# Kernel tuning notes

Measured on AMD Instinct MI355X. Metric: run time of the kernel, lower is better.

Reference implementation:

```python
import jax, jax.numpy as jnp
import numpy as np

D_MODEL = 1024
NUM_HEADS = 16
D_K = D_MODEL // NUM_HEADS


def setup_inputs() -> dict:
    key = jax.random.key(0)
    ks = jax.random.split(key, 5)
    B, S = 4, 2048
    scale = 1.0 / np.sqrt(D_MODEL)
    x = jax.random.normal(ks[0], (B, S, D_MODEL), dtype=jnp.float32)
    # Linear(d_model, d_model, bias=False) weights, stored as [out, in] like torch
    Wq = jax.random.normal(ks[1], (D_MODEL, D_MODEL), dtype=jnp.float32) * scale
    Wk = jax.random.normal(ks[2], (D_MODEL, D_MODEL), dtype=jnp.float32) * scale
    Wv = jax.random.normal(ks[3], (D_MODEL, D_MODEL), dtype=jnp.float32) * scale
    Wo = jax.random.normal(ks[4], (D_MODEL, D_MODEL), dtype=jnp.float32) * scale
    return {"x": x, "Wq": Wq, "Wk": Wk, "Wv": Wv, "Wo": Wo}


def reference(x, Wq, Wk, Wv, Wo):
    B, S, D = x.shape
    H, dk = NUM_HEADS, D_K
    # projections (torch Linear: x @ W.T)
    q = (x @ Wq.T).reshape(B, S, H, dk).transpose(0, 2, 1, 3)  # [B,H,S,dk]
    k = (x @ Wk.T).reshape(B, S, H, dk).transpose(0, 2, 1, 3)
    v = (x @ Wv.T).reshape(B, S, H, dk).transpose(0, 2, 1, 3)
    scores = jnp.einsum("bhqd,bhkd->bhqk", q, k) / jnp.sqrt(jnp.float32(dk))
    causal = jnp.triu(jnp.ones((S, S), dtype=bool), k=1)  # True above diagonal -> masked
    scores = jnp.where(causal[None, None], -jnp.inf, scores)
    attn = jax.nn.softmax(scores, axis=-1)
    out = jnp.einsum("bhqk,bhkd->bhqd", attn, v)  # [B,H,S,dk]
    out = out.transpose(0, 2, 1, 3).reshape(B, S, D)
    return out @ Wo.T
```

## Files before the change

### kernel.cpp

```cpp
#include <hip/hip_runtime.h>

typedef __bf16 bf16_t;
typedef __bf16 bf16x8 __attribute__((ext_vector_type(8)));
typedef __bf16 bf16x4 __attribute__((ext_vector_type(4)));
typedef float f32x4 __attribute__((ext_vector_type(4)));
typedef unsigned short u16x8 __attribute__((ext_vector_type(8)));

#define AS1C(p) ((const __attribute__((address_space(1))) void*)(p))
#define AS3(p) ((__attribute__((address_space(3))) void*)(p))
#define MM(a, b, c) __builtin_amdgcn_mfma_f32_16x16x32_bf16(a, b, c, 0, 0, 0)

__device__ __forceinline__ unsigned short f2b_rne(float f) {
  union { float f; unsigned u; } x; x.f = f;
  unsigned u = x.u;
  u += 0x7fffu + ((u >> 16) & 1u);
  return (unsigned short)(u >> 16);
}

__device__ __forceinline__ float fast_exp2(float x) {
  return __builtin_amdgcn_exp2f(x);
}

__global__ __launch_bounds__(256) void cast_all(const float* __restrict__ x,
                                                const float* __restrict__ w0,
                                                const float* __restrict__ w1,
                                                const float* __restrict__ w2,
                                                const float* __restrict__ w3,
                                                unsigned short* __restrict__ xout,
                                                unsigned short* __restrict__ wout) {
  int bid = blockIdx.x;
  const float* in;
  unsigned short* out;
  int base;
  if (bid < 4096) {
    in = x; out = xout; base = bid * 2048;
  } else {
    int widx = (bid - 4096) >> 9;
    in = (widx == 0) ? w0 : (widx == 1) ? w1 : (widx == 2) ? w2 : w3;
    out = wout + (size_t)widx * (1024u * 1024u);
    base = ((bid - 4096) & 511) * 2048;
  }
  int i = base + threadIdx.x * 8;
  const float4* p = reinterpret_cast<const float4*>(in + i);
  float4 a = p[0], b = p[1];
  u16x8 o;
  o[0] = f2b_rne(a.x); o[1] = f2b_rne(a.y); o[2] = f2b_rne(a.z); o[3] = f2b_rne(a.w);
  o[4] = f2b_rne(b.x); o[5] = f2b_rne(b.y); o[6] = f2b_rne(b.z); o[7] = f2b_rne(b.w);
  *reinterpret_cast<u16x8*>(out + i) = o;
}

template <int OUT_F32, int NJ>
__global__ __launch_bounds__(512, 4) void gemmk(const bf16_t* __restrict__ A,
                                                const bf16_t* __restrict__ Bm,
                                                void* __restrict__ C,
                                                int M, int N, int K, int lda,
                                                float scale, int qlim) {
  constexpr int BN = NJ * 64;
  constexpr int BUFE = (128 + BN) * 32;
  extern __shared__ bf16_t lds[];
  const int tid = threadIdx.x;
  const int w = tid >> 6, l = tid & 63;
  const int r = l & 15, kg = l >> 4;
  const int wm = (w >> 2) * 64;
  const int wn = (w & 3) * (NJ * 16);
  const int m0 = blockIdx.y * 128, n0 = blockIdx.x * BN;
  const int srow = w * 16 + (l >> 2);
  const int scol = (l & 3) * 8;
  const bf16_t* aS = A + (size_t)(m0 + srow) * lda + scol;
  const bf16_t* bS = Bm + (size_t)(n0 + srow) * K + scol;

  f32x4 acc[4][NJ] = {};

  auto STAGE = [&](bf16_t* sb, int kt) {
    __builtin_amdgcn_global_load_lds(AS1C(aS + kt * 32), AS3(sb + w * 512), 16, 0, 0);
    __builtin_amdgcn_global_load_lds(AS1C(bS + kt * 32), AS3(sb + 4096 + w * 512), 16, 0, 0);
    if (NJ == 4)
      __builtin_amdgcn_global_load_lds(AS1C(bS + (size_t)128 * K + kt * 32),
                                       AS3(sb + 8192 + w * 512), 16, 0, 0);
  };

  bf16_t* cur = lds;
  bf16_t* nxt = lds + BUFE;
  bf16_t* stg = lds + 2 * BUFE;

  STAGE(cur, 0);
  STAGE(nxt, 1);
  if (NJ == 4) asm volatile("s_waitcnt vmcnt(3)" ::: "memory");
  else         asm volatile("s_waitcnt vmcnt(2)" ::: "memory");
  __builtin_amdgcn_s_barrier();

  const int NT = K >> 5;
  for (int t = 0; t < NT; ++t) {
    bf16x8 AF[4], BF[NJ];
#pragma unroll
    for (int il = 0; il < 4; ++il)
      AF[il] = *reinterpret_cast<const bf16x8*>(cur + (wm + il * 16 + r) * 32 + kg * 8);
#pragma unroll
    for (int jl = 0; jl < NJ; ++jl)
      BF[jl] = *reinterpret_cast<const bf16x8*>(cur + 4096 + (wn + jl * 16 + r) * 32 + kg * 8);
    const int kt = (t + 2 < NT) ? t + 2 : t;
    STAGE(stg, kt);
    if (NJ == 4) asm volatile("s_waitcnt lgkmcnt(2)" ::: "memory");
    else         asm volatile("s_waitcnt lgkmcnt(1)" ::: "memory");
    __builtin_amdgcn_sched_barrier(0);
    __builtin_amdgcn_s_setprio(1);
#pragma unroll
    for (int il = 0; il < 4; ++il)
#pragma unroll
      for (int jl = 0; jl < NJ / 2; ++jl)
        acc[il][jl] = MM(AF[il], BF[jl], acc[il][jl]);
    __builtin_amdgcn_s_setprio(0);
    asm volatile("s_waitcnt lgkmcnt(0)" ::: "memory");
    __builtin_amdgcn_sched_barrier(0);
    __builtin_amdgcn_s_setprio(1);
#pragma unroll
    for (int il = 0; il < 4; ++il)
#pragma unroll
      for (int jl = NJ / 2; jl < NJ; ++jl)
        acc[il][jl] = MM(AF[il], BF[jl], acc[il][jl]);
    __builtin_amdgcn_s_setprio(0);
    if (NJ == 4) asm volatile("s_waitcnt vmcnt(3)" ::: "memory");
    else         asm volatile("s_waitcnt vmcnt(2)" ::: "memory");
    __builtin_amdgcn_s_barrier();
    bf16_t* tmp = cur; cur = nxt; nxt = stg; stg = tmp;
  }

#pragma unroll
  for (int il = 0; il < 4; ++il)
#pragma unroll
    for (int jl = 0; jl < NJ; ++jl) {
      const int row0 = m0 + wm + il * 16 + kg * 4;
      const int col = n0 + wn + jl * 16 + r;
      const float sc = (col < qlim) ? scale : 1.0f;
#pragma unroll
      for (int v = 0; v < 4; ++v) {
        float val = acc[il][jl][v] * sc;
        size_t idx = (size_t)(row0 + v) * N + col;
        if (OUT_F32) reinterpret_cast<float*>(C)[idx] = val;
        else reinterpret_cast<unsigned short*>(C)[idx] = f2b_rne(val);
      }
    }
}

__global__ __launch_bounds__(256) void transpose_v(const bf16_t* __restrict__ qkv,
                                                   bf16_t* __restrict__ vt) {
  __shared__ bf16_t Vs[64 * 72];
  const int t = threadIdx.x;
  const int s0 = blockIdx.x * 64;
  const int bh = blockIdx.y;
  const int b = bh >> 4, h = bh & 15;
  const size_t in_base = ((size_t)b * 2048 + s0) * 3072 + 2048 + h * 64;
#pragma unroll
  for (int c = 0; c < 2; ++c) {
    int chunk = c * 256 + t;
    int ss = chunk >> 3, dd = (chunk & 7) * 8;
    bf16x8 v = *reinterpret_cast<const bf16x8*>(qkv + in_base + (size_t)ss * 3072 + dd);
    *reinterpret_cast<bf16x8*>(Vs + ss * 72 + dd) = v;
  }
  __syncthreads();
  const size_t out_base = (size_t)bh * 64 * 2048 + s0;
#pragma unroll
  for (int c = 0; c < 2; ++c) {
    int chunk = c * 256 + t;
    int dd = chunk >> 3, ss = (chunk & 7) * 8;
    bf16x8 o;
#pragma unroll
    for (int j = 0; j < 8; ++j) o[j] = Vs[(ss + j) * 72 + dd];
    *reinterpret_cast<bf16x8*>(vt + out_base + (size_t)dd * 2048 + ss) = o;
  }
}

__global__ __launch_bounds__(512, 4) void flash_attn(const bf16_t* __restrict__ QKV,
                                                     const bf16_t* __restrict__ VT,
                                                     unsigned short* __restrict__ O,
                                                     int ostride) {
  __shared__ bf16_t Ks[2][64 * 72];
  __shared__ bf16_t Vts[2][64 * 72];
  __shared__ bf16_t Pl[8][2][16 * 68];
  const int tid = threadIdx.x;
  const int lane = tid & 63, wave = tid >> 6;
  const int r = lane & 15, kg = lane >> 4;
  const int bh = blockIdx.x;
  const int y = blockIdx.y;
  const int pair = (y < 4) ? y : 11 - y;
  const int b = bh >> 4, h = bh & 15;
  const size_t qkv_row0 = (size_t)b * 2048 * 3072;
  const int qcol = h * 64, kcol = 1024 + h * 64;
  const size_t vt_base = (size_t)bh * 64 * 2048;
  const size_t o_row0 = (size_t)b * 2048 * ostride;
  const int ocol = h * 64;
  const int srr = tid >> 3, scc = (tid & 7) * 8;

  const int q0L = pair * 128, q0H = (15 - pair) * 128;
  const int qrowL = q0L + wave * 16 + r, qrowH = q0H + wave * 16 + r;
  const int tmaxL = (q0L + wave * 16 + 15) >> 6;
  const int tmaxH = (q0H + wave * 16 + 15) >> 6;
  const int NT = 32 - 2 * pair;

  const size_t qoffL = qkv_row0 + (size_t)qrowL * 3072 + qcol;
  const size_t qoffH = qkv_row0 + (size_t)qrowH * 3072 + qcol;
  bf16x8 qfL0 = *reinterpret_cast<const bf16x8*>(QKV + qoffL + kg * 8);
  bf16x8 qfL1 = *reinterpret_cast<const bf16x8*>(QKV + qoffL + 32 + kg * 8);
  bf16x8 qfH0 = *reinterpret_cast<const bf16x8*>(QKV + qoffH + kg * 8);
  bf16x8 qfH1 = *reinterpret_cast<const bf16x8*>(QKV + qoffH + 32 + kg * 8);

  f32x4 oaccL[4] = {}, oaccH[4] = {};
  float mL = -3e30f, lL = 0.f, mH = -3e30f, lH = 0.f;

  bf16x8 gk = *reinterpret_cast<const bf16x8*>(QKV + qkv_row0 + (size_t)srr * 3072 + kcol + scc);
  bf16x8 gv = *reinterpret_cast<const bf16x8*>(VT + vt_base + (size_t)srr * 2048 + scc);

  for (int t = 0; t < NT; ++t) {
    const int buf = t & 1;
    *reinterpret_cast<bf16x8*>(&Ks[buf][srr * 72 + scc]) = gk;
    *reinterpret_cast<bf16x8*>(&Vts[buf][srr * 72 + scc]) = gv;
    __syncthreads();
    if (t + 1 < NT) {
      const int kv1 = (t + 1) * 64;
      gk = *reinterpret_cast<const bf16x8*>(QKV + qkv_row0 + (size_t)(kv1 + srr) * 3072 + kcol + scc);
      gv = *reinterpret_cast<const bf16x8*>(VT + vt_base + (size_t)srr * 2048 + kv1 + scc);
    }
    if (t > tmaxH) continue;

    const int kv0 = t * 64;
    const bool doL = (t <= tmaxL);

    bf16x8 kf[4][2];
#pragma unroll
    for (int nt = 0; nt < 4; ++nt) {
      kf[nt][0] = *reinterpret_cast<const bf16x8*>(&Ks[buf][(nt * 16 + r) * 72 + kg * 8]);
      kf[nt][1] = *reinterpret_cast<const bf16x8*>(&Ks[buf][(nt * 16 + r) * 72 + 32 + kg * 8]);
    }
    float valsL[16], valsH[16];
    __builtin_amdgcn_s_setprio(1);
    if (doL) {
#pragma unroll
      for (int nt = 0; nt < 4; ++nt) {
        f32x4 sL = {};
        sL = MM(kf[nt][0], qfL0, sL);
        sL = MM(kf[nt][1], qfL1, sL);
#pragma unroll
        for (int v = 0; v < 4; ++v) valsL[nt * 4 + v] = sL[v];
      }
    }
#pragma unroll
    for (int nt = 0; nt < 4; ++nt) {
      f32x4 sH = {};
      sH = MM(kf[nt][0], qfH0, sH);
      sH = MM(kf[nt][1], qfH1, sH);
#pragma unroll
      for (int v = 0; v < 4; ++v) valsH[nt * 4 + v] = sH[v];
    }
    __builtin_amdgcn_s_setprio(0);

    if (doL) {
      if (t == tmaxL) {
#pragma unroll
        for (int nt = 0; nt < 4; ++nt)
#pragma unroll
          for (int v = 0; v < 4; ++v)
            if (kv0 + nt * 16 + kg * 4 + v > qrowL) valsL[nt * 4 + v] = -3e30f;
      }
      float a0 = fmaxf(fmaxf(valsL[0], valsL[1]), valsL[2]);
      float a1 = fmaxf(fmaxf(valsL[3], valsL[4]), valsL[5]);
      float a2 = fmaxf(fmaxf(valsL[6], valsL[7]), valsL[8]);
      float a3 = fmaxf(fmaxf(valsL[9], valsL[10]), valsL[11]);
      float a4 = fmaxf(fmaxf(valsL[12], valsL[13]), valsL[14]);
      float pmax = fmaxf(fmaxf(fmaxf(a0, a1), fmaxf(a2, a3)), fmaxf(a4, valsL[15]));
      if (!__all(pmax <= mL + 8.0f)) {
        pmax = fmaxf(pmax, __shfl_xor(pmax, 16));
        pmax = fmaxf(pmax, __shfl_xor(pmax, 32));
        const float m_new = fmaxf(mL, pmax);
        const float alpha = fast_exp2(mL - m_new);
        lL *= alpha;
        f32x4 al;
#pragma unroll
        for (int v = 0; v < 4; ++v) al[v] = __shfl(alpha, kg * 4 + v);
#pragma unroll
        for (int dt = 0; dt < 4; ++dt)
#pragma unroll
          for (int v = 0; v < 4; ++v) oaccL[dt][v] *= al[v];
        mL = m_new;
      }
#pragma unroll
      for (int ii = 0; ii < 16; ++ii) {
        float p = fast_exp2(valsL[ii] - mL);
        valsL[ii] = p;
        lL += p;
      }
#pragma unroll
      for (int nt = 0; nt < 4; ++nt) {
        bf16x4 pb;
#pragma unroll
        for (int v = 0; v < 4; ++v) pb[v] = (bf16_t)valsL[nt * 4 + v];
        *reinterpret_cast<bf16x4*>(&Pl[wave][0][r * 68 + nt * 16 + kg * 4]) = pb;
      }
      bf16x8 pa0 = *reinterpret_cast<const bf16x8*>(&Pl[wave][0][r * 68 + kg * 8]);
      bf16x8 pa1 = *reinterpret_cast<const bf16x8*>(&Pl[wave][0][r * 68 + 32 + kg * 8]);
#pragma unroll
      for (int dt = 0; dt < 4; ++dt) {
        bf16x8 vb0 = *reinterpret_cast<const bf16x8*>(&Vts[buf][(dt * 16 + r) * 72 + kg * 8]);
        bf16x8 vb1 = *reinterpret_cast<const bf16x8*>(&Vts[buf][(dt * 16 + r) * 72 + 32 + kg * 8]);
        oaccL[dt] = MM(pa0, vb0, oaccL[dt]);
        oaccL[dt] = MM(pa1, vb1, oaccL[dt]);
      }
    }

    {
      if (t == tmaxH) {
#pragma unroll
        for (int nt = 0; nt < 4; ++nt)
#pragma unroll
          for (int v = 0; v < 4; ++v)
            if (kv0 + nt * 16 + kg * 4 + v > qrowH) valsH[nt * 4 + v] = -3e30f;
      }
      float a0 = fmaxf(fmaxf(valsH[0], valsH[1]), valsH[2]);
      float a1 = fmaxf(fmaxf(valsH[3], valsH[4]), valsH[5]);
      float a2 = fmaxf(fmaxf(valsH[6], valsH[7]), valsH[8]);
      float a3 = fmaxf(fmaxf(valsH[9], valsH[10]), valsH[11]);
      float a4 = fmaxf(fmaxf(valsH[12], valsH[13]), valsH[14]);
      float pmax = fmaxf(fmaxf(fmaxf(a0, a1), fmaxf(a2, a3)), fmaxf(a4, valsH[15]));
      if (!__all(pmax <= mH + 8.0f)) {
        pmax = fmaxf(pmax, __shfl_xor(pmax, 16));
        pmax = fmaxf(pmax, __shfl_xor(pmax, 32));
        const float m_new = fmaxf(mH, pmax);
        const float alpha = fast_exp2(mH - m_new);
        lH *= alpha;
        f32x4 al;
#pragma unroll
        for (int v = 0; v < 4; ++v) al[v] = __shfl(alpha, kg * 4 + v);
#pragma unroll
        for (int dt = 0; dt < 4; ++dt)
#pragma unroll
          for (int v = 0; v < 4; ++v) oaccH[dt][v] *= al[v];
        mH = m_new;
      }
#pragma unroll
      for (int ii = 0; ii < 16; ++ii) {
        float p = fast_exp2(valsH[ii] - mH);
        valsH[ii] = p;
        lH += p;
      }
#pragma unroll
      for (int nt = 0; nt < 4; ++nt) {
        bf16x4 pb;
#pragma unroll
        for (int v = 0; v < 4; ++v) pb[v] = (bf16_t)valsH[nt * 4 + v];
        *reinterpret_cast<bf16x4*>(&Pl[wave][1][r * 68 + nt * 16 + kg * 4]) = pb;
      }
      bf16x8 pa0 = *reinterpret_cast<const bf16x8*>(&Pl[wave][1][r * 68 + kg * 8]);
      bf16x8 pa1 = *reinterpret_cast<const bf16x8*>(&Pl[wave][1][r * 68 + 32 + kg * 8]);
      __builtin_amdgcn_s_setprio(1);
#pragma unroll
      for (int dt = 0; dt < 4; ++dt) {
        bf16x8 vb0 = *reinterpret_cast<const bf16x8*>(&Vts[buf][(dt * 16 + r) * 72 + kg * 8]);
        bf16x8 vb1 = *reinterpret_cast<const bf16x8*>(&Vts[buf][(dt * 16 + r) * 72 + 32 + kg * 8]);
        oaccH[dt] = MM(pa0, vb0, oaccH[dt]);
        oaccH[dt] = MM(pa1, vb1, oaccH[dt]);
      }
      __builtin_amdgcn_s_setprio(0);
    }
  }

  {
    float l_row = lL;
    l_row += __shfl_xor(l_row, 16);
    l_row += __shfl_xor(l_row, 32);
    const float linv = 1.0f / l_row;
    f32x4 il;
#pragma unroll
    for (int v = 0; v < 4; ++v) il[v] = __shfl(linv, kg * 4 + v);
    const size_t orow0 = o_row0 + (size_t)(q0L + wave * 16) * ostride + ocol;
#pragma unroll
    for (int dt = 0; dt < 4; ++dt) {
      const int d = dt * 16 + r;
#pragma unroll
      for (int v = 0; v < 4; ++v)
        O[orow0 + (size_t)(kg * 4 + v) * ostride + d] = f2b_rne(oaccL[dt][v] * il[v]);
    }
  }
  {
    float l_row = lH;
    l_row += __shfl_xor(l_row, 16);
    l_row += __shfl_xor(l_row, 32);
    const float linv = 1.0f / l_row;
    f32x4 il;
#pragma unroll
    for (int v = 0; v < 4; ++v) il[v] = __shfl(linv, kg * 4 + v);
    const size_t orow0 = o_row0 + (size_t)(q0H + wave * 16) * ostride + ocol;
#pragma unroll
    for (int dt = 0; dt < 4; ++dt) {
      const int d = dt * 16 + r;
#pragma unroll
      for (int v = 0; v < 4; ++v)
        O[orow0 + (size_t)(kg * 4 + v) * ostride + d] = f2b_rne(oaccH[dt][v] * il[v]);
    }
  }
}

extern "C" void kernel_launch(void* const* d_in, const int* in_sizes, int n_in,
                              void* d_out, int out_size, void* d_ws, size_t ws_size,
                              hipStream_t stream) {
  const float* x  = (const float*)d_in[0];
  const float* Wq = (const float*)d_in[1];
  const float* Wk = (const float*)d_in[2];
  const float* Wv = (const float*)d_in[3];
  const float* Wo = (const float*)d_in[4];

  char* ws = (char*)d_ws;
  bf16_t* xb  = (bf16_t*)(ws);
  bf16_t* wqb = (bf16_t*)(ws + (16u << 20));
  bf16_t* wob = (bf16_t*)(ws + (22u << 20));
  bf16_t* qkv = (bf16_t*)(ws + (24u << 20));
  bf16_t* vt  = (bf16_t*)(ws);

  hipFuncSetAttribute(reinterpret_cast<const void*>(&gemmk<0, 4>),
                      hipFuncAttributeMaxDynamicSharedMemorySize, 73728);
  hipFuncSetAttribute(reinterpret_cast<const void*>(&gemmk<1, 2>),
                      hipFuncAttributeMaxDynamicSharedMemorySize, 49152);

  cast_all<<<4096 + 2048, 256, 0, stream>>>(x, Wq, Wk, Wv, Wo,
                                            (unsigned short*)xb, (unsigned short*)wqb);

  gemmk<0, 4><<<dim3(3072 / 256, 8192 / 128), 512, 73728, stream>>>(
      xb, wqb, qkv, 8192, 3072, 1024, 1024, 0.18033688011112042f, 1024);

  transpose_v<<<dim3(2048 / 64, 64), 256, 0, stream>>>(qkv, vt);

  flash_attn<<<dim3(64, 8), 512, 0, stream>>>(qkv, vt, (unsigned short*)qkv, 3072);

  gemmk<1, 2><<<dim3(1024 / 128, 8192 / 128), 512, 49152, stream>>>(
      qkv, wob, d_out, 8192, 1024, 1024, 3072, 1.0f, 0);
}
```

Before: 172.9 us.

## Fuse V transpose into QKV GEMM epilogue and hoist V fragment loads

Result: slower. 219.4 us (+26.9%).

```diff
diff --git a/kernel.cpp b/kernel.cpp
--- a/kernel.cpp
+++ b/kernel.cpp
@@ -5,6 +5,7 @@
 typedef __bf16 bf16x4 __attribute__((ext_vector_type(4)));
 typedef float f32x4 __attribute__((ext_vector_type(4)));
 typedef unsigned short u16x8 __attribute__((ext_vector_type(8)));
+typedef unsigned short u16x4 __attribute__((ext_vector_type(4)));
 
 #define AS1C(p) ((const __attribute__((address_space(1))) void*)(p))
 #define AS3(p) ((__attribute__((address_space(3))) void*)(p))
@@ -53,7 +54,8 @@
 __global__ __launch_bounds__(512, 4) void gemmk(const bf16_t* __restrict__ A,
                                                 const bf16_t* __restrict__ Bm,
                                                 void* __restrict__ C,
-                                                int M, int N, int K, int lda,
+                                                bf16_t* __restrict__ vt,
+                                                int M, int ldc, int K, int lda,
                                                 float scale, int qlim) {
   constexpr int BN = NJ * 64;
   constexpr int BUFE = (128 + BN) * 32;
@@ -125,6 +127,22 @@
     bf16_t* tmp = cur; cur = nxt; nxt = stg; stg = tmp;
   }
 
+  if (!OUT_F32 && vt && n0 >= 2048) {
+#pragma unroll
+    for (int il = 0; il < 4; ++il)
+#pragma unroll
+      for (int jl = 0; jl < NJ; ++jl) {
+        const int row0 = m0 + wm + il * 16 + kg * 4;
+        const int vc = n0 + wn + jl * 16 + r - 2048;
+        const int hh = vc >> 6, dd = vc & 63;
+        const int bb = row0 >> 11, ss = row0 & 2047;
+        u16x4 pb;
+#pragma unroll
+        for (int v = 0; v < 4; ++v) pb[v] = f2b_rne(acc[il][jl][v]);
+        *reinterpret_cast<u16x4*>(vt + ((size_t)((bb * 16 + hh) * 64 + dd) << 11) + ss) = pb;
+      }
+    return;
+  }
 #pragma unroll
   for (int il = 0; il < 4; ++il)
 #pragma unroll
@@ -135,42 +153,14 @@
 #pragma unroll
       for (int v = 0; v < 4; ++v) {
         float val = acc[il][jl][v] * sc;
-        size_t idx = (size_t)(row0 + v) * N + col;
+        size_t idx = (size_t)(row0 + v) * ldc + col;
         if (OUT_F32) reinterpret_cast<float*>(C)[idx] = val;
         else reinterpret_cast<unsigned short*>(C)[idx] = f2b_rne(val);
       }
     }
 }
 
-__global__ __launch_bounds__(256) void transpose_v(const bf16_t* __restrict__ qkv,
-                                                   bf16_t* __restrict__ vt) {
-  __shared__ bf16_t Vs[64 * 72];
-  const int t = threadIdx.x;
-  const int s0 = blockIdx.x * 64;
-  const int bh = blockIdx.y;
-  const int b = bh >> 4, h = bh & 15;
-  const size_t in_base = ((size_t)b * 2048 + s0) * 3072 + 2048 + h * 64;
-#pragma unroll
-  for (int c = 0; c < 2; ++c) {
-    int chunk = c * 256 + t;
-    int ss = chunk >> 3, dd = (chunk & 7) * 8;
-    bf16x8 v = *reinterpret_cast<const bf16x8*>(qkv + in_base + (size_t)ss * 3072 + dd);
-    *reinterpret_cast<bf16x8*>(Vs + ss * 72 + dd) = v;
-  }
-  __syncthreads();
-  const size_t out_base = (size_t)bh * 64 * 2048 + s0;
-#pragma unroll
-  for (int c = 0; c < 2; ++c) {
-    int chunk = c * 256 + t;
-    int dd = chunk >> 3, ss = (chunk & 7) * 8;
-    bf16x8 o;
-#pragma unroll
-    for (int j = 0; j < 8; ++j) o[j] = Vs[(ss + j) * 72 + dd];
-    *reinterpret_cast<bf16x8*>(vt + out_base + (size_t)dd * 2048 + ss) = o;
-  }
-}
-
-__global__ __launch_bounds__(512, 4) void flash_attn(const bf16_t* __restrict__ QKV,
+__global__ __launch_bounds__(512, 4) void flash_attn(const bf16_t* __restrict__ QK,
                                                      const bf16_t* __restrict__ VT,
                                                      unsigned short* __restrict__ O,
                                                      int ostride) {
@@ -184,7 +174,7 @@
   const int y = blockIdx.y;
   const int pair = (y < 4) ? y : 11 - y;
   const int b = bh >> 4, h = bh & 15;
-  const size_t qkv_row0 = (size_t)b * 2048 * 3072;
+  const size_t qk_row0 = (size_t)b * 2048 * 2048;
   const int qcol = h * 64, kcol = 1024 + h * 64;
   const size_t vt_base = (size_t)bh * 64 * 2048;
   const size_t o_row0 = (size_t)b * 2048 * ostride;
@@ -197,17 +187,17 @@
   const int tmaxH = (q0H + wave * 16 + 15) >> 6;
   const int NT = 32 - 2 * pair;
 
-  const size_t qoffL = qkv_row0 + (size_t)qrowL * 3072 + qcol;
-  const size_t qoffH = qkv_row0 + (size_t)qrowH * 3072 + qcol;
-  bf16x8 qfL0 = *reinterpret_cast<const bf16x8*>(QKV + qoffL + kg * 8);
-  bf16x8 qfL1 = *reinterpret_cast<const bf16x8*>(QKV + qoffL + 32 + kg * 8);
-  bf16x8 qfH0 = *reinterpret_cast<const bf16x8*>(QKV + qoffH + kg * 8);
-  bf16x8 qfH1 = *reinterpret_cast<const bf16x8*>(QKV + qoffH + 32 + kg * 8);
+  const size_t qoffL = qk_row0 + (size_t)qrowL * 2048 + qcol;
+  const size_t qoffH = qk_row0 + (size_t)qrowH * 2048 + qcol;
+  bf16x8 qfL0 = *reinterpret_cast<const bf16x8*>(QK + qoffL + kg * 8);
+  bf16x8 qfL1 = *reinterpret_cast<const bf16x8*>(QK + qoffL + 32 + kg * 8);
+  bf16x8 qfH0 = *reinterpret_cast<const bf16x8*>(QK + qoffH + kg * 8);
+  bf16x8 qfH1 = *reinterpret_cast<const bf16x8*>(QK + qoffH + 32 + kg * 8);
 
   f32x4 oaccL[4] = {}, oaccH[4] = {};
   float mL = -3e30f, lL = 0.f, mH = -3e30f, lH = 0.f;
 
-  bf16x8 gk = *reinterpret_cast<const bf16x8*>(QKV + qkv_row0 + (size_t)srr * 3072 + kcol + scc);
+  bf16x8 gk = *reinterpret_cast<const bf16x8*>(QK + qk_row0 + (size_t)srr * 2048 + kcol + scc);
   bf16x8 gv = *reinterpret_cast<const bf16x8*>(VT + vt_base + (size_t)srr * 2048 + scc);
 
   for (int t = 0; t < NT; ++t) {
@@ -217,7 +207,7 @@
     __syncthreads();
     if (t + 1 < NT) {
       const int kv1 = (t + 1) * 64;
-      gk = *reinterpret_cast<const bf16x8*>(QKV + qkv_row0 + (size_t)(kv1 + srr) * 3072 + kcol + scc);
+      gk = *reinterpret_cast<const bf16x8*>(QK + qk_row0 + (size_t)(kv1 + srr) * 2048 + kcol + scc);
       gv = *reinterpret_cast<const bf16x8*>(VT + vt_base + (size_t)srr * 2048 + kv1 + scc);
     }
     if (t > tmaxH) continue;
@@ -252,6 +242,13 @@
       for (int v = 0; v < 4; ++v) valsH[nt * 4 + v] = sH[v];
     }
     __builtin_amdgcn_s_setprio(0);
+
+    bf16x8 vf[4][2];
+#pragma unroll
+    for (int dt = 0; dt < 4; ++dt) {
+      vf[dt][0] = *reinterpret_cast<const bf16x8*>(&Vts[buf][(dt * 16 + r) * 72 + kg * 8]);
+      vf[dt][1] = *reinterpret_cast<const bf16x8*>(&Vts[buf][(dt * 16 + r) * 72 + 32 + kg * 8]);
+    }
 
     if (doL) {
       if (t == tmaxL) {
@@ -299,10 +296,8 @@
       bf16x8 pa1 = *reinterpret_cast<const bf16x8*>(&Pl[wave][0][r * 68 + 32 + kg * 8]);
 #pragma unroll
       for (int dt = 0; dt < 4; ++dt) {
-        bf16x8 vb0 = *reinterpret_cast<const bf16x8*>(&Vts[buf][(dt * 16 + r) * 72 + kg * 8]);
-        bf16x8 vb1 = *reinterpret_cast<const bf16x8*>(&Vts[buf][(dt * 16 + r) * 72 + 32 + kg * 8]);
-        oaccL[dt] = MM(pa0, vb0, oaccL[dt]);
-        oaccL[dt] = MM(pa1, vb1, oaccL[dt]);
+        oaccL[dt] = MM(pa0, vf[dt][0], oaccL[dt]);
+        oaccL[dt] = MM(pa1, vf[dt][1], oaccL[dt]);
       }
     }
 
@@ -353,10 +348,8 @@
       __builtin_amdgcn_s_setprio(1);
 #pragma unroll
       for (int dt = 0; dt < 4; ++dt) {
-        bf16x8 vb0 = *reinterpret_cast<const bf16x8*>(&Vts[buf][(dt * 16 + r) * 72 + kg * 8]);
-        bf16x8 vb1 = *reinterpret_cast<const bf16x8*>(&Vts[buf][(dt * 16 + r) * 72 + 32 + kg * 8]);
-        oaccH[dt] = MM(pa0, vb0, oaccH[dt]);
-        oaccH[dt] = MM(pa1, vb1, oaccH[dt]);
+        oaccH[dt] = MM(pa0, vf[dt][0], oaccH[dt]);
+        oaccH[dt] = MM(pa1, vf[dt][1], oaccH[dt]);
       }
       __builtin_amdgcn_s_setprio(0);
     }
@@ -411,8 +404,8 @@
   bf16_t* xb  = (bf16_t*)(ws);
   bf16_t* wqb = (bf16_t*)(ws + (16u << 20));
   bf16_t* wob = (bf16_t*)(ws + (22u << 20));
-  bf16_t* qkv = (bf16_t*)(ws + (24u << 20));
-  bf16_t* vt  = (bf16_t*)(ws);
+  bf16_t* qk  = (bf16_t*)(ws + (24u << 20));
+  bf16_t* vt  = (bf16_t*)(ws + (56u << 20));
 
   hipFuncSetAttribute(reinterpret_cast<const void*>(&gemmk<0, 4>),
                       hipFuncAttributeMaxDynamicSharedMemorySize, 73728);
@@ -423,12 +416,10 @@
                                             (unsigned short*)xb, (unsigned short*)wqb);
 
   gemmk<0, 4><<<dim3(3072 / 256, 8192 / 128), 512, 73728, stream>>>(
-      xb, wqb, qkv, 8192, 3072, 1024, 1024, 0.18033688011112042f, 1024);
-
-  transpose_v<<<dim3(2048 / 64, 64), 256, 0, stream>>>(qkv, vt);
-
-  flash_attn<<<dim3(64, 8), 512, 0, stream>>>(qkv, vt, (unsigned short*)qkv, 3072);
+      xb, wqb, qk, vt, 8192, 2048, 1024, 1024, 0.18033688011112042f, 1024);
+
+  flash_attn<<<dim3(64, 8), 512, 0, stream>>>(qk, vt, (unsigned short*)qk, 2048);
 
   gemmk<1, 2><<<dim3(1024 / 128, 8192 / 128), 512, 49152, stream>>>(
-      qkv, wob, d_out, 8192, 1024, 1024, 3072, 1.0f, 0);
-}
+      qk, wob, d_out, nullptr, 8192, 1024, 1024, 2048, 1.0f, 0);
+}
```
